# Performance work log

Hardware: AMD Instinct MI355X
Metric: run time of the kernel (lower is better)

## Reference

```python
import jax, jax.numpy as jnp
import numpy as np

DIM = 1024
HEADS = 16
BLK = 129
DK = 64
DV = 64
B = 4
N = BLK * 32  # 4128


def setup_inputs() -> dict:
    key = jax.random.key(0)
    ks = jax.random.split(key, 6)
    inner_k = HEADS * DK
    inner_v = HEADS * DV
    s = 1.0 / np.sqrt(DIM)
    x = jax.random.normal(ks[0], (B, N, DIM), dtype=jnp.float32)
    Wq = jax.random.normal(ks[1], (inner_k, DIM), dtype=jnp.float32) * s
    Wk = jax.random.normal(ks[2], (inner_k, DIM), dtype=jnp.float32) * s
    Wv = jax.random.normal(ks[3], (inner_v, DIM), dtype=jnp.float32) * s
    Wo = jax.random.normal(ks[4], (DIM, inner_v), dtype=jnp.float32) * (1.0 / np.sqrt(inner_v))
    bo = jax.random.normal(ks[5], (DIM,), dtype=jnp.float32) * 0.01
    return {"x": x, "Wq": Wq, "Wk": Wk, "Wv": Wv, "Wo": Wo, "bo": bo}


def reference(x, Wq, Wk, Wv, Wo, bo):
    Bsz, Nlen, D = x.shape
    nb = Nlen // BLK
    scale = 1.0 / np.sqrt(DK)
    # projections (Linear without bias: x @ W.T)
    q = (x @ Wq.T).reshape(Bsz, nb, BLK, HEADS, DK)
    k = (x @ Wk.T).reshape(Bsz, nb, BLK, HEADS, DK)
    v = (x @ Wv.T).reshape(Bsz, nb, BLK, HEADS, DV)
    # block-local attention: each block attends within itself
    scores = jnp.einsum('bnqhd,bnkhd->bnhqk', q, k) * scale  # [B,nb,H,BLK,BLK]
    attn = jax.nn.softmax(scores, axis=-1)
    out_blk = jnp.einsum('bnhqk,bnkhd->bnhqd', attn, v)  # [B,nb,H,BLK,DV]
    # global attention among the first token of each block
    qg = q[:, :, 0]  # [B,nb,H,DK]
    kg = k[:, :, 0]
    vg = v[:, :, 0]
    sg = jnp.einsum('bqhd,bkhd->bhqk', qg, kg) * scale  # [B,H,nb,nb]
    ag = jax.nn.softmax(sg, axis=-1)
    out_g = jnp.einsum('bhqk,bkhd->bqhd', ag, vg)  # [B,nb,H,DV]
    # add global output onto position 0 of each block
    out_blk = out_blk.at[:, :, :, 0, :].add(out_g.transpose(0, 1, 2, 3).swapaxes(2, 2))  # out_g already [B,nb,H,DV]
    # reassemble to [B,N,H*DV]
    out = out_blk.transpose(0, 1, 3, 2, 4).reshape(Bsz, Nlen, HEADS * DV)
    return out @ Wo.T + bo
```

## Files before the change

### kernel.cpp

```cpp
#include <hip/hip_runtime.h>

typedef unsigned short u16;
typedef __attribute__((ext_vector_type(8))) __bf16 bf16x8;
typedef __attribute__((ext_vector_type(4))) float f32x4;
typedef __attribute__((ext_vector_type(8))) u16 u16x8;
typedef __attribute__((ext_vector_type(4))) u16 u16x4;

#define DIMSZ 1024
#define HEADS 16
#define BLKSZ 129
#define NBLK 32
#define NTOK (BLKSZ * NBLK)
#define BATCH 4
#define MROWS (BATCH * NTOK)

#define MFMA __builtin_amdgcn_mfma_f32_16x16x32_bf16

#define SSTR 152
#define KSTR 72

#define NKT 32
#define NPH 32

__device__ __forceinline__ float bf2f(u16 u) {
  return __uint_as_float(((unsigned)u) << 16);
}
__device__ __forceinline__ u16 f2bf(float f) {
  unsigned u = __float_as_uint(f);
  u += 0x7FFFu + ((u >> 16) & 1u);
  return (u16)(u >> 16);
}

#define GLD16(ldsp, gp) __builtin_amdgcn_global_load_lds( \
    (const __attribute__((address_space(1))) void*)(gp),   \
    (__attribute__((address_space(3))) void*)(ldsp), 16, 0, 0)

__global__ __launch_bounds__(256) void cast_in(
    const float* __restrict__ x, const float* __restrict__ wq,
    const float* __restrict__ wk, const float* __restrict__ wv,
    u16* __restrict__ x16, u16* __restrict__ w16)
{
  const int nx = MROWS * DIMSZ, nw = DIMSZ * DIMSZ;
  int i = (blockIdx.x * 256 + threadIdx.x) * 4;
  const float* src;
  u16* dst;
  int j;
  if (i < nx) { src = x; dst = x16; j = i; }
  else {
    int k = i - nx;
    dst = w16; j = k;
    src = (k < nw) ? wq : (k < 2 * nw ? wk : wv);
    j = (k < nw) ? k : (k < 2 * nw ? k - nw : k - 2 * nw);
  }
  float4 f = *(const float4*)(src + j);
  u16x4 o = { f2bf(f.x), f2bf(f.y), f2bf(f.z), f2bf(f.w) };
  *(u16x4*)(dst + (i < nx ? j : (i - nx))) = o;
}

__global__ __launch_bounds__(256) void cast_f32_bf16(
    const float* __restrict__ in, u16* __restrict__ out, int n)
{
  int i = (blockIdx.x * 256 + threadIdx.x) * 4;
  if (i < n) {
    float4 f = *(const float4*)(in + i);
    u16x4 o = { f2bf(f.x), f2bf(f.y), f2bf(f.z), f2bf(f.w) };
    *(u16x4*)(out + i) = o;
  }
}

__device__ __forceinline__ int xcd_swz(int bid, int nwg) {
  const int xcd = bid & 7, l = bid >> 3;
  const int q = nwg >> 3, r = nwg & 7;
  return (xcd < r ? xcd * (q + 1) : r * (q + 1) + (xcd - r) * q) + l;
}

__device__ __forceinline__ void stage_pair(u16* slot, const u16* gA1,
                                           const u16* gB1, int k0, int tid) {
  GLD16(slot + tid * 8, gA1 + k0);
  GLD16(slot + 4096 + tid * 8, gA1 + 128 * DIMSZ + k0);
  GLD16(slot + 8192 + tid * 8, gB1 + k0);
  GLD16(slot + 12288 + tid * 8, gB1 + 128 * DIMSZ + k0);
}

#define RD8(slot, row, sw) (*(const bf16x8*)&(slot)[(row) * 32 + (sw)])

__global__ __launch_bounds__(512, 1) void gemm_qkv(
    const u16* __restrict__ A, const u16* __restrict__ B,
    u16* __restrict__ Cq, u16* __restrict__ Ck, u16* __restrict__ Cv)
{
  __shared__ u16 sm[4][16384];
  const int tid = threadIdx.x;
  const int lane = tid & 63, w = tid >> 6;
  const int qd = lane >> 4, l15 = lane & 15;
  const int wm = (w >> 2) * 128, wn = (w & 3) * 64;
  const int qdsw = (qd ^ ((l15 >> 1) & 3)) * 8;

  f32x4 acc[8][4];
#pragma unroll
  for (int mi = 0; mi < 8; ++mi)
#pragma unroll
    for (int ni = 0; ni < 4; ++ni)
      acc[mi][ni] = (f32x4){0.f, 0.f, 0.f, 0.f};

  const int wg = xcd_swz(blockIdx.x, 65 * 12);
  const int nt = wg % 12, mt = wg / 12;
  const int m0 = mt * 256, n0 = nt * 256;

  const int srow = tid >> 2;
  const int schk = (tid & 3) ^ ((tid >> 3) & 3);
  const u16* gA1 = A + (size_t)(m0 + srow) * DIMSZ + schk * 8;
  const u16* gB1 = B + (size_t)(n0 + srow) * DIMSZ + schk * 8;

  stage_pair(sm[0], gA1, gB1, 0, tid);
  stage_pair(sm[1], gA1, gB1, 32, tid);
  stage_pair(sm[2], gA1, gB1, 64, tid);
  asm volatile("s_waitcnt vmcnt(4)" ::: "memory");
  __builtin_amdgcn_s_barrier();
  __builtin_amdgcn_sched_barrier(0);

  bf16x8 afLa[4], bva[4], afLb[4], bvb[4], afH[4];
#pragma unroll
  for (int mi = 0; mi < 4; ++mi) afLa[mi] = RD8(sm[0], wm + mi * 16 + l15, qdsw);
#pragma unroll
  for (int ni = 0; ni < 4; ++ni) bva[ni] = RD8(sm[0] + 8192, wn + ni * 16 + l15, qdsw);

#define QSTEP(T, AC, BC, AN, BN)                                              \
  {                                                                           \
    const u16* slc = sm[(T) & 3];                                             \
    if ((T) + 3 < NPH)                                                        \
      stage_pair(sm[((T) + 3) & 3], gA1, gB1, ((T) + 3) * 32, tid);           \
    _Pragma("unroll")                                                         \
    for (int mi = 0; mi < 4; ++mi)                                            \
      afH[mi] = RD8(slc, wm + 64 + mi * 16 + l15, qdsw);                      \
    _Pragma("unroll")                                                         \
    for (int mi = 0; mi < 4; ++mi)                                            \
      _Pragma("unroll")                                                       \
      for (int ni = 0; ni < 4; ++ni)                                          \
        acc[mi][ni] = MFMA(AC[mi], BC[ni], acc[mi][ni], 0, 0, 0);             \
    if ((T) + 1 < NPH) {                                                      \
      const u16* sln = sm[((T) + 1) & 3];                                     \
      _Pragma("unroll")                                                       \
      for (int mi = 0; mi < 4; ++mi)                                          \
        AN[mi] = RD8(sln, wm + mi * 16 + l15, qdsw);                          \
      _Pragma("unroll")                                                       \
      for (int ni = 0; ni < 4; ++ni)                                          \
        BN[ni] = RD8(sln + 8192, wn + ni * 16 + l15, qdsw);                   \
    }                                                                         \
    _Pragma("unroll")                                                         \
    for (int mi = 0; mi < 4; ++mi)                                            \
      _Pragma("unroll")                                                       \
      for (int ni = 0; ni < 4; ++ni)                                          \
        acc[mi + 4][ni] = MFMA(afH[mi], BC[ni], acc[mi + 4][ni], 0, 0, 0);    \
    __builtin_amdgcn_sched_barrier(0);                                        \
    if ((T) + 3 < NPH) {                                                      \
      asm volatile("s_waitcnt vmcnt(4)" ::: "memory");                        \
    } else {                                                                  \
      asm volatile("s_waitcnt vmcnt(0)" ::: "memory");                        \
    }                                                                         \
    __builtin_amdgcn_s_barrier();                                             \
    __builtin_amdgcn_sched_barrier(0);                                        \
  }

  for (int t = 0; t < NPH; t += 2) {
    QSTEP(t, afLa, bva, afLb, bvb);
    QSTEP(t + 1, afLb, bvb, afLa, bva);
  }
#undef QSTEP

  u16* C = nt < 4 ? Cq : (nt < 8 ? Ck : Cv);
  const int c0 = (nt & 3) * 256;
#pragma unroll
  for (int mi = 0; mi < 8; ++mi)
#pragma unroll
    for (int ni = 0; ni < 4; ++ni) {
      const int row0 = m0 + wm + mi * 16 + qd * 4;
      const int col  = c0 + wn + ni * 16 + l15;
#pragma unroll
      for (int r = 0; r < 4; ++r)
        if (row0 + r < MROWS)
          C[(size_t)(row0 + r) * DIMSZ + col] = f2bf(acc[mi][ni][r]);
    }
}

__device__ __forceinline__ void stage_sq(u16* slot, const u16* gA,
                                         const u16* gB, int tid) {
  GLD16(slot + tid * 8, gA);
  GLD16(slot + 2048 + tid * 8, gA + 64 * DIMSZ);
  GLD16(slot + 4096 + tid * 8, gB);
  GLD16(slot + 6144 + tid * 8, gB + 64 * DIMSZ);
}

__device__ __forceinline__ void gemm_pipe_sq(
    const u16* __restrict__ A, const u16* __restrict__ Bm,
    int m0, int n0, int tid, u16 (*sm)[8192], f32x4 (*acc)[4])
{
  const int lane = tid & 63, w = tid >> 6;
  const int qd = lane >> 4, l15 = lane & 15;
  const int wm = (w >> 1) * 64, wn = (w & 1) * 64;
  const int qdsw = (qd ^ ((l15 >> 1) & 3)) * 8;

  const int srow = tid >> 2;
  const int schk = (tid & 3) ^ ((tid >> 3) & 3);
  const u16* gA = A + (size_t)(m0 + srow) * DIMSZ + schk * 8;
  const u16* gB = Bm + (size_t)(n0 + srow) * DIMSZ + schk * 8;

  u16 *p0 = sm[0], *p1 = sm[1], *p2 = sm[2];

  stage_sq(p0, gA, gB, tid);
  stage_sq(p1, gA + 32, gB + 32, tid);
  asm volatile("s_waitcnt vmcnt(4)" ::: "memory");
  __builtin_amdgcn_s_barrier();
  __builtin_amdgcn_sched_barrier(0);

  for (int t = 0; t < NKT; ++t) {
    if (t + 2 < NKT)
      stage_sq(p2, gA + (t + 2) * 32, gB + (t + 2) * 32, tid);

    bf16x8 af[4], bv[4];
#pragma unroll
    for (int mi = 0; mi < 4; ++mi)
      af[mi] = *(const bf16x8*)&p0[(wm + mi * 16 + l15) * 32 + qdsw];
#pragma unroll
    for (int ni = 0; ni < 4; ++ni)
      bv[ni] = *(const bf16x8*)&p0[4096 + (wn + ni * 16 + l15) * 32 + qdsw];

    __builtin_amdgcn_s_setprio(1);
#pragma unroll
    for (int mi = 0; mi < 4; ++mi)
#pragma unroll
      for (int ni = 0; ni < 4; ++ni)
        acc[mi][ni] = MFMA(af[mi], bv[ni], acc[mi][ni], 0, 0, 0);
    __builtin_amdgcn_s_setprio(0);

    __builtin_amdgcn_sched_barrier(0);
    if (t + 2 < NKT) {
      asm volatile("s_waitcnt vmcnt(4)" ::: "memory");
    } else {
      asm volatile("s_waitcnt vmcnt(0)" ::: "memory");
    }
    __builtin_amdgcn_s_barrier();
    __builtin_amdgcn_sched_barrier(0);

    u16* tmp = p0; p0 = p1; p1 = p2; p2 = tmp;
  }
}

__global__ __launch_bounds__(256, 3) void gemm_out(
    const u16* __restrict__ A, const u16* __restrict__ B,
    float* __restrict__ C, const float* __restrict__ bias)
{
  __shared__ u16 sm[3][8192];
  const int tid = threadIdx.x;
  f32x4 acc[4][4];
#pragma unroll
  for (int mi = 0; mi < 4; ++mi)
#pragma unroll
    for (int ni = 0; ni < 4; ++ni)
      acc[mi][ni] = (f32x4){0.f, 0.f, 0.f, 0.f};

  const int wg = xcd_swz(blockIdx.x, 129 * 8);
  const int nt = wg & 7, mt = wg >> 3;
  const int m0 = mt * 128, n0 = nt * 128;

  gemm_pipe_sq(A, B, m0, n0, tid, sm, acc);

  const int lane = tid & 63, w = tid >> 6;
  const int qd = lane >> 4, l15 = lane & 15;
  const int wm = (w >> 1) * 64, wn = (w & 1) * 64;
#pragma unroll
  for (int mi = 0; mi < 4; ++mi)
#pragma unroll
    for (int ni = 0; ni < 4; ++ni) {
      const int row0 = m0 + wm + mi * 16 + qd * 4;
      const int col  = n0 + wn + ni * 16 + l15;
      float badd = bias[col];
#pragma unroll
      for (int r = 0; r < 4; ++r)
        C[(size_t)(row0 + r) * DIMSZ + col] = acc[mi][ni][r] + badd;
    }
}

__global__ __launch_bounds__(256) void global_attn(
    const u16* __restrict__ q, const u16* __restrict__ k,
    const u16* __restrict__ v, float* __restrict__ g)
{
  __shared__ float sQ[NBLK * 64];
  __shared__ float sKT[64 * NBLK];
  __shared__ float sV[NBLK * 64];
  __shared__ float sp[4][NBLK];
  const int b = blockIdx.x >> 4, h = blockIdx.x & 15;
  const int tid = threadIdx.x, lane = tid & 63, w = tid >> 6;

  for (int idx = tid; idx < NBLK * 64; idx += 256) {
    int j = idx >> 6, d = idx & 63;
    size_t off = ((size_t)(b * NTOK + j * BLKSZ)) * DIMSZ + h * 64 + d;
    sQ[idx] = bf2f(q[off]);
    sKT[d * NBLK + j] = bf2f(k[off]);
    sV[idx] = bf2f(v[off]);
  }
  __syncthreads();

  for (int i = w; i < NBLK; i += 4) {
    float s = -3.0e38f;
    if (lane < 32) {
      float acc = 0.f;
      for (int d = 0; d < 64; ++d) acc += sQ[i * 64 + d] * sKT[d * NBLK + lane];
      s = acc * 0.125f;
    }
    float m = s;
    for (int t = 1; t < 64; t <<= 1) m = fmaxf(m, __shfl_xor(m, t));
    float e = (lane < 32) ? __expf(s - m) : 0.f;
    float sum = e;
    for (int t = 1; t < 64; t <<= 1) sum += __shfl_xor(sum, t);
    if (lane < 32) sp[w][lane] = e / sum;
    asm volatile("s_waitcnt lgkmcnt(0)" ::: "memory");
    float acc = 0.f;
    for (int jj = 0; jj < NBLK; ++jj) acc += sp[w][jj] * sV[jj * 64 + lane];
    g[(((size_t)b * NBLK + i) * HEADS + h) * 64 + lane] = acc;
  }
}

__global__ __launch_bounds__(512) void block_attn(
    const u16* q, const u16* __restrict__ k,
    const u16* __restrict__ v, const float* __restrict__ g,
    u16* ao)
{
  __shared__ u16 sS[144 * SSTR];
  __shared__ u16 sKV[144 * KSTR];
  const int b = blockIdx.x, blk = blockIdx.y, h = blockIdx.z;
  const int tid = threadIdx.x, lane = tid & 63, w = tid >> 6;
  const int qd = lane >> 4, l15 = lane & 15;
  const int h64 = h * 64;
  const size_t row_base = (size_t)b * NTOK + (size_t)blk * BLKSZ;
  const f32x4 zero4 = {0.f, 0.f, 0.f, 0.f};

  {
    const u16x8 zero8 = {0, 0, 0, 0, 0, 0, 0, 0};
    for (int c = tid; c < 144 * 8; c += 512) {
      int row = c >> 3, cc = c & 7;
      u16x8 val = zero8;
      if (row < BLKSZ)
        val = *(const u16x8*)(k + (row_base + row) * DIMSZ + h64 + cc * 8);
      *(u16x8*)&sKV[row * KSTR + cc * 8] = val;
    }
  }
  __syncthreads();

  {
    const int tbeg = w * 10;
    const int tend = (w == 7) ? 81 : tbeg + 10;
    int cur_mt = -1;
    bf16x8 qf0, qf1;
    for (int t = tbeg; t < tend; ++t) {
      int mt = t / 9, nt = t - mt * 9;
      if (mt != cur_mt) {
        cur_mt = mt;
        int qrow = mt * 16 + l15;
        if (qrow > 128) qrow = 128;
        const u16* qp = q + (row_base + qrow) * DIMSZ + h64;
        qf0 = *(const bf16x8*)(qp + qd * 8);
        qf1 = *(const bf16x8*)(qp + 32 + qd * 8);
      }
      bf16x8 kf0 = *(const bf16x8*)&sKV[(nt * 16 + l15) * KSTR + qd * 8];
      bf16x8 kf1 = *(const bf16x8*)&sKV[(nt * 16 + l15) * KSTR + 32 + qd * 8];
      f32x4 c = zero4;
      c = MFMA(qf0, kf0, c, 0, 0, 0);
      c = MFMA(qf1, kf1, c, 0, 0, 0);
      int r0 = mt * 16 + qd * 4, col = nt * 16 + l15;
#pragma unroll
      for (int r = 0; r < 4; ++r)
        sS[(r0 + r) * SSTR + col] = f2bf(c[r] * 0.125f);
    }
  }
  __syncthreads();

  {
    int c = tid;
    int p = c >> 3, cc = c & 7;
    u16x8 v0 = *(const u16x8*)(v + (row_base + 2 * p) * DIMSZ + h64 + cc * 8);
    u16x8 v1 = *(const u16x8*)(v + (row_base + 2 * p + 1) * DIMSZ + h64 + cc * 8);
#pragma unroll
    for (int jj = 0; jj < 8; ++jj) {
      unsigned pack = (unsigned)v0[jj] | ((unsigned)v1[jj] << 16);
      *(unsigned*)&sKV[(cc * 8 + jj) * SSTR + 2 * p] = pack;
    }
    if (tid < 8) {
      u16x8 vl = *(const u16x8*)(v + (row_base + 128) * DIMSZ + h64 + tid * 8);
#pragma unroll
      for (int jj = 0; jj < 8; ++jj)
        sKV[(tid * 8 + jj) * SSTR + 128] = vl[jj];
    }
  }

  for (int row = w; row < BLKSZ; row += 8) {
    float x1 = bf2f(sS[row * SSTR + lane]);
    float x2 = bf2f(sS[row * SSTR + 64 + lane]);
    float x3 = (lane == 0) ? bf2f(sS[row * SSTR + 128]) : -3.0e38f;
    float m = fmaxf(fmaxf(x1, x2), x3);
    for (int t = 1; t < 64; t <<= 1) m = fmaxf(m, __shfl_xor(m, t));
    float e1 = __expf(x1 - m), e2 = __expf(x2 - m);
    float e3 = (lane == 0) ? __expf(x3 - m) : 0.f;
    float s = e1 + e2 + e3;
    for (int t = 1; t < 64; t <<= 1) s += __shfl_xor(s, t);
    float inv = 1.f / s;
    sS[row * SSTR + lane] = f2bf(e1 * inv);
    sS[row * SSTR + 64 + lane] = f2bf(e2 * inv);
    if (lane == 0) sS[row * SSTR + 128] = f2bf(e3 * inv);
  }
  __syncthreads();

  for (int t = w; t < 36; t += 8) {
    int mt = t >> 2, nt = t & 3;
    f32x4 c = zero4;
#pragma unroll
    for (int kk = 0; kk < 128; kk += 32) {
      bf16x8 pf = *(const bf16x8*)&sS[(mt * 16 + l15) * SSTR + kk + qd * 8];
      bf16x8 vf = *(const bf16x8*)&sKV[(nt * 16 + l15) * SSTR + kk + qd * 8];
      c = MFMA(pf, vf, c, 0, 0, 0);
    }
    int dv = nt * 16 + l15;
    float v128 = bf2f(sKV[dv * SSTR + 128]);
    int r0 = mt * 16 + qd * 4;
#pragma unroll
    for (int r = 0; r < 4; ++r) {
      int row = r0 + r;
      if (row < BLKSZ) {
        float p128 = bf2f(sS[row * SSTR + 128]);
        float val = c[r] + p128 * v128;
        if (row == 0)
          val += g[(((size_t)b * NBLK + blk) * HEADS + h) * 64 + dv];
        ao[(row_base + row) * DIMSZ + h64 + dv] = f2bf(val);
      }
    }
  }
}

extern "C" void kernel_launch(void* const* d_in, const int* in_sizes, int n_in,
                              void* d_out, int out_size, void* d_ws, size_t ws_size,
                              hipStream_t stream) {
  const float* x  = (const float*)d_in[0];
  const float* Wq = (const float*)d_in[1];
  const float* Wk = (const float*)d_in[2];
  const float* Wv = (const float*)d_in[3];
  const float* Wo = (const float*)d_in[4];
  const float* bo = (const float*)d_in[5];
  float* out = (float*)d_out;

  char* ws = (char*)d_ws;
  const size_t xb = (size_t)MROWS * DIMSZ * sizeof(u16);
  float* gb     = (float*)ws;
  u16*   qb     = (u16*)(ws + (1u << 20));
  u16*   x16    = (u16*)(ws + (1u << 20) + xb);
  u16*   Wqkv16 = (u16*)(ws + (1u << 20) + 2 * xb);
  u16*   Wo16   = x16;
  u16*   kb     = (u16*)d_out;
  u16*   vb     = (u16*)d_out + (size_t)MROWS * DIMSZ;

  const int nx = MROWS * DIMSZ;
  const int nw = DIMSZ * DIMSZ;
  cast_in<<<(nx + 3 * nw) / 1024, 256, 0, stream>>>(x, Wq, Wk, Wv, x16, Wqkv16);

  gemm_qkv<<<dim3(65 * 12), 512, 0, stream>>>(x16, Wqkv16, qb, kb, vb);

  cast_f32_bf16<<<nw / 1024, 256, 0, stream>>>(Wo, Wo16, nw);

  global_attn<<<dim3(BATCH * HEADS), 256, 0, stream>>>(qb, kb, vb, gb);
  block_attn<<<dim3(BATCH, NBLK, HEADS), 512, 0, stream>>>(qb, kb, vb, gb, qb);
  gemm_out<<<dim3(129 * 8), 256, 0, stream>>>(qb, Wo16, out, bo);
}
```

Measured before the change: 394.5 us.

## Fuse global attention and softmax into the block attention kernel

Removes the separate global_attn kernel. In its place, warp 0 of each block_attn workgroup computes that block's global-token output into shared memory while the other warps stage V. The QK^T scores are now kept in registers and the row softmax runs there with 16-lane shuffles, so unnormalised scores no longer make a round trip through LDS. The sS row stride is also changed from 152 to 154. The trade-offs are higher register pressure and redundant strided global loads of first-token K and V in every workgroup.

```diff
diff --git a/kernel.cpp b/kernel.cpp
--- a/kernel.cpp
+++ b/kernel.cpp
@@ -16,7 +16,7 @@
 
 #define MFMA __builtin_amdgcn_mfma_f32_16x16x32_bf16
 
-#define SSTR 152
+#define SSTR 154
 #define KSTR 72
 
 #define NKT 32
@@ -280,53 +280,13 @@
     }
 }
 
-__global__ __launch_bounds__(256) void global_attn(
-    const u16* __restrict__ q, const u16* __restrict__ k,
-    const u16* __restrict__ v, float* __restrict__ g)
-{
-  __shared__ float sQ[NBLK * 64];
-  __shared__ float sKT[64 * NBLK];
-  __shared__ float sV[NBLK * 64];
-  __shared__ float sp[4][NBLK];
-  const int b = blockIdx.x >> 4, h = blockIdx.x & 15;
-  const int tid = threadIdx.x, lane = tid & 63, w = tid >> 6;
-
-  for (int idx = tid; idx < NBLK * 64; idx += 256) {
-    int j = idx >> 6, d = idx & 63;
-    size_t off = ((size_t)(b * NTOK + j * BLKSZ)) * DIMSZ + h * 64 + d;
-    sQ[idx] = bf2f(q[off]);
-    sKT[d * NBLK + j] = bf2f(k[off]);
-    sV[idx] = bf2f(v[off]);
-  }
-  __syncthreads();
-
-  for (int i = w; i < NBLK; i += 4) {
-    float s = -3.0e38f;
-    if (lane < 32) {
-      float acc = 0.f;
-      for (int d = 0; d < 64; ++d) acc += sQ[i * 64 + d] * sKT[d * NBLK + lane];
-      s = acc * 0.125f;
-    }
-    float m = s;
-    for (int t = 1; t < 64; t <<= 1) m = fmaxf(m, __shfl_xor(m, t));
-    float e = (lane < 32) ? __expf(s - m) : 0.f;
-    float sum = e;
-    for (int t = 1; t < 64; t <<= 1) sum += __shfl_xor(sum, t);
-    if (lane < 32) sp[w][lane] = e / sum;
-    asm volatile("s_waitcnt lgkmcnt(0)" ::: "memory");
-    float acc = 0.f;
-    for (int jj = 0; jj < NBLK; ++jj) acc += sp[w][jj] * sV[jj * 64 + lane];
-    g[(((size_t)b * NBLK + i) * HEADS + h) * 64 + lane] = acc;
-  }
-}
-
 __global__ __launch_bounds__(512) void block_attn(
     const u16* q, const u16* __restrict__ k,
-    const u16* __restrict__ v, const float* __restrict__ g,
-    u16* ao)
+    const u16* __restrict__ v, u16* ao)
 {
   __shared__ u16 sS[144 * SSTR];
   __shared__ u16 sKV[144 * KSTR];
+  __shared__ float sG[64];
   const int b = blockIdx.x, blk = blockIdx.y, h = blockIdx.z;
   const int tid = threadIdx.x, lane = tid & 63, w = tid >> 6;
   const int qd = lane >> 4, l15 = lane & 15;
@@ -347,65 +307,98 @@
   __syncthreads();
 
   {
-    const int tbeg = w * 10;
-    const int tend = (w == 7) ? 81 : tbeg + 10;
-    int cur_mt = -1;
-    bf16x8 qf0, qf1;
-    for (int t = tbeg; t < tend; ++t) {
-      int mt = t / 9, nt = t - mt * 9;
-      if (mt != cur_mt) {
-        cur_mt = mt;
-        int qrow = mt * 16 + l15;
-        if (qrow > 128) qrow = 128;
-        const u16* qp = q + (row_base + qrow) * DIMSZ + h64;
-        qf0 = *(const bf16x8*)(qp + qd * 8);
-        qf1 = *(const bf16x8*)(qp + 32 + qd * 8);
+    const int npass = (w == 7) ? 2 : 1;
+    for (int pass = 0; pass < npass; ++pass) {
+      const int mt = pass ? 8 : w;
+      int qrow = mt * 16 + l15;
+      if (qrow > 128) qrow = 128;
+      const u16* qp = q + (row_base + qrow) * DIMSZ + h64;
+      bf16x8 qf0 = *(const bf16x8*)(qp + qd * 8);
+      bf16x8 qf1 = *(const bf16x8*)(qp + 32 + qd * 8);
+
+      f32x4 c[9];
+#pragma unroll
+      for (int nt = 0; nt < 9; ++nt) {
+        bf16x8 kf0 = *(const bf16x8*)&sKV[(nt * 16 + l15) * KSTR + qd * 8];
+        bf16x8 kf1 = *(const bf16x8*)&sKV[(nt * 16 + l15) * KSTR + 32 + qd * 8];
+        f32x4 cc0 = MFMA(qf0, kf0, zero4, 0, 0, 0);
+        c[nt] = MFMA(qf1, kf1, cc0, 0, 0, 0);
+#pragma unroll
+        for (int r = 0; r < 4; ++r) c[nt][r] *= 0.125f;
       }
-      bf16x8 kf0 = *(const bf16x8*)&sKV[(nt * 16 + l15) * KSTR + qd * 8];
-      bf16x8 kf1 = *(const bf16x8*)&sKV[(nt * 16 + l15) * KSTR + 32 + qd * 8];
-      f32x4 c = zero4;
-      c = MFMA(qf0, kf0, c, 0, 0, 0);
-      c = MFMA(qf1, kf1, c, 0, 0, 0);
-      int r0 = mt * 16 + qd * 4, col = nt * 16 + l15;
-#pragma unroll
-      for (int r = 0; r < 4; ++r)
-        sS[(r0 + r) * SSTR + col] = f2bf(c[r] * 0.125f);
+
+#pragma unroll
+      for (int r = 0; r < 4; ++r) {
+        float m = (l15 == 0) ? c[8][r] : -3.0e38f;
+#pragma unroll
+        for (int nt = 0; nt < 8; ++nt) m = fmaxf(m, c[nt][r]);
+        for (int t = 1; t < 16; t <<= 1) m = fmaxf(m, __shfl_xor(m, t));
+        float e[8], sum;
+        float e8 = (l15 == 0) ? __expf(c[8][r] - m) : 0.f;
+        sum = e8;
+#pragma unroll
+        for (int nt = 0; nt < 8; ++nt) { e[nt] = __expf(c[nt][r] - m); sum += e[nt]; }
+        for (int t = 1; t < 16; t <<= 1) sum += __shfl_xor(sum, t);
+        float inv = 1.f / sum;
+        int row = mt * 16 + qd * 4 + r;
+        if (row <= 128) {
+#pragma unroll
+          for (int nt = 0; nt < 8; ++nt)
+            sS[row * SSTR + nt * 16 + l15] = f2bf(e[nt] * inv);
+          if (l15 == 0) sS[row * SSTR + 128] = f2bf(e8 * inv);
+        }
+      }
     }
   }
   __syncthreads();
 
-  {
-    int c = tid;
-    int p = c >> 3, cc = c & 7;
-    u16x8 v0 = *(const u16x8*)(v + (row_base + 2 * p) * DIMSZ + h64 + cc * 8);
-    u16x8 v1 = *(const u16x8*)(v + (row_base + 2 * p + 1) * DIMSZ + h64 + cc * 8);
-#pragma unroll
-    for (int jj = 0; jj < 8; ++jj) {
-      unsigned pack = (unsigned)v0[jj] | ((unsigned)v1[jj] << 16);
-      *(unsigned*)&sKV[(cc * 8 + jj) * SSTR + 2 * p] = pack;
-    }
-    if (tid < 8) {
-      u16x8 vl = *(const u16x8*)(v + (row_base + 128) * DIMSZ + h64 + tid * 8);
+  if (w > 0) {
+    int c = tid - 64;
+#pragma unroll 1
+    for (int rep = 0; rep < 2; ++rep) {
+      if (rep == 1) { if (tid >= 128) break; c = 448 + (tid - 64); }
+      int p = c >> 3, cc = c & 7;
+      u16x8 v0 = *(const u16x8*)(v + (row_base + 2 * p) * DIMSZ + h64 + cc * 8);
+      u16x8 v1 = *(const u16x8*)(v + (row_base + 2 * p + 1) * DIMSZ + h64 + cc * 8);
+#pragma unroll
+      for (int jj = 0; jj < 8; ++jj) {
+        unsigned pack = (unsigned)v0[jj] | ((unsigned)v1[jj] << 16);
+        *(unsigned*)&sKV[(cc * 8 + jj) * SSTR + 2 * p] = pack;
+      }
+    }
+    if (tid >= 128 && tid < 136) {
+      int cc = tid - 128;
+      u16x8 vl = *(const u16x8*)(v + (row_base + 128) * DIMSZ + h64 + cc * 8);
 #pragma unroll
       for (int jj = 0; jj < 8; ++jj)
-        sKV[(tid * 8 + jj) * SSTR + 128] = vl[jj];
-    }
-  }
-
-  for (int row = w; row < BLKSZ; row += 8) {
-    float x1 = bf2f(sS[row * SSTR + lane]);
-    float x2 = bf2f(sS[row * SSTR + 64 + lane]);
-    float x3 = (lane == 0) ? bf2f(sS[row * SSTR + 128]) : -3.0e38f;
-    float m = fmaxf(fmaxf(x1, x2), x3);
+        sKV[(cc * 8 + jj) * SSTR + 128] = vl[jj];
+    }
+  } else {
+    const u16* qgp = q + row_base * DIMSZ + h64;
+    const u16* kgp = k + ((size_t)b * NTOK + (size_t)(lane & 31) * BLKSZ) * DIMSZ + h64;
+    float acc = 0.f;
+#pragma unroll
+    for (int d0 = 0; d0 < 8; ++d0) {
+      u16x8 qc = *(const u16x8*)(qgp + d0 * 8);
+      u16x8 kc = *(const u16x8*)(kgp + d0 * 8);
+#pragma unroll
+      for (int j = 0; j < 8; ++j)
+        acc += bf2f(qc[j]) * bf2f(kc[j]);
+    }
+    float s = (lane < 32) ? acc * 0.125f : -3.0e38f;
+    float m = s;
     for (int t = 1; t < 64; t <<= 1) m = fmaxf(m, __shfl_xor(m, t));
-    float e1 = __expf(x1 - m), e2 = __expf(x2 - m);
-    float e3 = (lane == 0) ? __expf(x3 - m) : 0.f;
-    float s = e1 + e2 + e3;
-    for (int t = 1; t < 64; t <<= 1) s += __shfl_xor(s, t);
-    float inv = 1.f / s;
-    sS[row * SSTR + lane] = f2bf(e1 * inv);
-    sS[row * SSTR + 64 + lane] = f2bf(e2 * inv);
-    if (lane == 0) sS[row * SSTR + 128] = f2bf(e3 * inv);
+    float e = (lane < 32) ? __expf(s - m) : 0.f;
+    float sum = e;
+    for (int t = 1; t < 64; t <<= 1) sum += __shfl_xor(sum, t);
+    float p = e / sum;
+    float accO = 0.f;
+    for (int j = 0; j < 32; ++j) {
+      float pj = __shfl(p, j);
+      const u16* vr = v + ((size_t)b * NTOK + (size_t)j * BLKSZ) * DIMSZ + h64;
+      accO += pj * bf2f(vr[lane]);
+    }
+    sG[lane] = accO;
   }
   __syncthreads();
 
@@ -428,7 +421,7 @@
         float p128 = bf2f(sS[row * SSTR + 128]);
         float val = c[r] + p128 * v128;
         if (row == 0)
-          val += g[(((size_t)b * NBLK + blk) * HEADS + h) * 64 + dv];
+          val += sG[dv];
         ao[(row_base + row) * DIMSZ + h64 + dv] = f2bf(val);
       }
     }
@@ -448,7 +441,6 @@
 
   char* ws = (char*)d_ws;
   const size_t xb = (size_t)MROWS * DIMSZ * sizeof(u16);
-  float* gb     = (float*)ws;
   u16*   qb     = (u16*)(ws + (1u << 20));
   u16*   x16    = (u16*)(ws + (1u << 20) + xb);
   u16*   Wqkv16 = (u16*)(ws + (1u << 20) + 2 * xb);
@@ -464,7 +456,6 @@
 
   cast_f32_bf16<<<nw / 1024, 256, 0, stream>>>(Wo, Wo16, nw);
 
-  global_attn<<<dim3(BATCH * HEADS), 256, 0, stream>>>(qb, kb, vb, gb);
-  block_attn<<<dim3(BATCH, NBLK, HEADS), 512, 0, stream>>>(qb, kb, vb, gb, qb);
+  block_attn<<<dim3(BATCH, NBLK, HEADS), 512, 0, stream>>>(qb, kb, vb, qb);
   gemm_out<<<dim3(129 * 8), 256, 0, stream>>>(qb, Wo16, out, bo);
 }
```

After: 396.7 us. About the same (+0.5%).
